# Kernel optimization log

Measured on AMD Instinct MI355X. Metric: run time of the kernel, lower is better.

## Reference

```python
import jax, jax.numpy as jnp
import numpy as np

DIM = 2048
DIM_HEAD = 64
NUM_HEADS = 32
FFN_INNER = 4 * DIM  # 8192
ATTN_INNER = NUM_HEADS * DIM_HEAD  # 2048
IN_WIDTH = FFN_INNER * 2 + 3 * ATTN_INNER  # 22528
OUT_IN = FFN_INNER + DIM  # 10240
B, S = 1, 2048


def setup_inputs() -> dict:
    key = jax.random.key(0)
    k0, k1, k2 = jax.random.split(key, 3)
    x = jax.random.normal(k0, (B, S, DIM), dtype=jnp.float32)
    W_in = jax.random.normal(k1, (DIM, IN_WIDTH), dtype=jnp.float32) * (DIM ** -0.5)
    W_out = jax.random.normal(k2, (OUT_IN, DIM), dtype=jnp.float32) * (OUT_IN ** -0.5)
    ln_w = jnp.ones((DIM,), dtype=jnp.float32)
    ln_b = jnp.zeros((DIM,), dtype=jnp.float32)
    return {"x": x, "ln_w": ln_w, "ln_b": ln_b, "W_in": W_in, "W_out": W_out}


def _layernorm(x, w, b, eps=1e-5):
    mu = jnp.mean(x, axis=-1, keepdims=True)
    var = jnp.mean(jnp.square(x - mu), axis=-1, keepdims=True)
    return (x - mu) * jax.lax.rsqrt(var + eps) * w + b


def reference(x, ln_w, ln_b, W_in, W_out):
    b, s, _ = x.shape
    h = _layernorm(x, ln_w, ln_b)
    res = h @ W_in  # [b, s, IN_WIDTH]
    q = res[..., :ATTN_INNER]
    k = res[..., ATTN_INNER:2 * ATTN_INNER]
    v = res[..., 2 * ATTN_INNER:3 * ATTN_INNER]
    ffn_input = res[..., 3 * ATTN_INNER:3 * ATTN_INNER + FFN_INNER]
    # b s (h d) -> b h s d
    q = q.reshape(b, s, NUM_HEADS, DIM_HEAD).transpose(0, 2, 1, 3)
    k = k.reshape(b, s, NUM_HEADS, DIM_HEAD).transpose(0, 2, 1, 3)
    v = v.reshape(b, s, NUM_HEADS, DIM_HEAD).transpose(0, 2, 1, 3)
    q = q * (DIM_HEAD ** -0.5)
    sim = jnp.einsum('bhsd,bhnd->bhsn', q, k)  # [b, h, s, s]
    causal = jnp.triu(jnp.ones((s, s), dtype=bool), k=1)
    sim = jnp.where(causal, -jnp.finfo(sim.dtype).max, sim)
    attn = jax.nn.softmax(sim, axis=-1)
    attn_out = jnp.einsum('bhsn,bhnd->bhsd', attn, v)
    attn_out = attn_out.transpose(0, 2, 1, 3).reshape(b, s, ATTN_INNER)
    concat_input = jnp.concatenate([attn_out, ffn_input], axis=-1)  # [b, s, OUT_IN]
    return concat_input @ W_out
```

## Files before the change

### kernel.cpp

```cpp
#include <hip/hip_runtime.h>
#include <stdint.h>

typedef __bf16 bf16x8 __attribute__((ext_vector_type(8)));
typedef float f32x4 __attribute__((ext_vector_type(4)));
typedef uint16_t u16x4 __attribute__((ext_vector_type(4)));
typedef uint16_t u16x8 __attribute__((ext_vector_type(8)));

#define LOG2E 1.4426950408889634f

__device__ __forceinline__ uint16_t f2bf(float f) {
  union { float f; uint32_t u; } v; v.f = f;
  return (uint16_t)((v.u + 0x7fffu + ((v.u >> 16) & 1u)) >> 16);
}

__device__ __forceinline__ void gload_lds16(const void* g, void* l) {
  __builtin_amdgcn_global_load_lds(
      (const __attribute__((address_space(1))) void*)g,
      (__attribute__((address_space(3))) void*)l, 16, 0, 0);
}

__device__ __forceinline__ f32x4 mfma16(bf16x8 a, bf16x8 b, f32x4 c) {
  return __builtin_amdgcn_mfma_f32_16x16x32_bf16(a, b, c, 0, 0, 0);
}

__global__ __launch_bounds__(256) void ln_kernel(const float* __restrict__ x,
                                                 const float* __restrict__ g,
                                                 const float* __restrict__ bta,
                                                 uint16_t* __restrict__ h) {
  const int row = blockIdx.x;
  const int t = threadIdx.x;
  const float* xr = x + (size_t)row * 2048 + t * 8;
  float4 v0 = *(const float4*)xr;
  float4 v1 = *(const float4*)(xr + 4);
  float s = v0.x + v0.y + v0.z + v0.w + v1.x + v1.y + v1.z + v1.w;
  float q = v0.x*v0.x + v0.y*v0.y + v0.z*v0.z + v0.w*v0.w
          + v1.x*v1.x + v1.y*v1.y + v1.z*v1.z + v1.w*v1.w;
  #pragma unroll
  for (int m = 1; m < 64; m <<= 1) {
    s += __shfl_xor(s, m);
    q += __shfl_xor(q, m);
  }
  __shared__ float ps[4], pq[4];
  const int wid = t >> 6, lane = t & 63;
  if (lane == 0) { ps[wid] = s; pq[wid] = q; }
  __syncthreads();
  s = ps[0] + ps[1] + ps[2] + ps[3];
  q = pq[0] + pq[1] + pq[2] + pq[3];
  const float mu = s * (1.0f / 2048.0f);
  const float var = q * (1.0f / 2048.0f) - mu * mu;
  const float rs = rsqrtf(var + 1e-5f);
  float4 w0 = *(const float4*)(g + t * 8);
  float4 w1 = *(const float4*)(g + t * 8 + 4);
  float4 b0 = *(const float4*)(bta + t * 8);
  float4 b1 = *(const float4*)(bta + t * 8 + 4);
  u16x8 o;
  o[0] = f2bf((v0.x - mu) * rs * w0.x + b0.x);
  o[1] = f2bf((v0.y - mu) * rs * w0.y + b0.y);
  o[2] = f2bf((v0.z - mu) * rs * w0.z + b0.z);
  o[3] = f2bf((v0.w - mu) * rs * w0.w + b0.w);
  o[4] = f2bf((v1.x - mu) * rs * w1.x + b1.x);
  o[5] = f2bf((v1.y - mu) * rs * w1.y + b1.y);
  o[6] = f2bf((v1.z - mu) * rs * w1.z + b1.z);
  o[7] = f2bf((v1.w - mu) * rs * w1.w + b1.w);
  *(u16x8*)(h + (size_t)row * 2048 + t * 8) = o;
}

__global__ __launch_bounds__(256) void transpose_w(const float* __restrict__ in,
                                                   uint16_t* __restrict__ out,
                                                   int R, int ldin,
                                                   int scale_cols, float scale) {
  __shared__ uint16_t tile[64][65];
  const int c0 = blockIdx.x * 64;
  const int r0 = blockIdx.y * 64;
  const int t = threadIdx.x;
  const int cc = (t & 15) * 4;
  const int rb = t >> 4;
  #pragma unroll
  for (int p = 0; p < 4; ++p) {
    const int r = rb + p * 16;
    const float4 v = *(const float4*)(in + (size_t)(r0 + r) * ldin + c0 + cc);
    const float m0 = (c0 + cc + 0) < scale_cols ? scale : 1.0f;
    const float m1 = (c0 + cc + 1) < scale_cols ? scale : 1.0f;
    const float m2 = (c0 + cc + 2) < scale_cols ? scale : 1.0f;
    const float m3 = (c0 + cc + 3) < scale_cols ? scale : 1.0f;
    tile[r][cc + 0] = f2bf(v.x * m0);
    tile[r][cc + 1] = f2bf(v.y * m1);
    tile[r][cc + 2] = f2bf(v.z * m2);
    tile[r][cc + 3] = f2bf(v.w * m3);
  }
  __syncthreads();
  #pragma unroll
  for (int p = 0; p < 4; ++p) {
    const int oc = rb + p * 16;
    u16x4 ov;
    ov.x = tile[cc + 0][oc];
    ov.y = tile[cc + 1][oc];
    ov.z = tile[cc + 2][oc];
    ov.w = tile[cc + 3][oc];
    *(u16x4*)(out + (size_t)(c0 + oc) * R + r0 + cc) = ov;
  }
}

__global__ __launch_bounds__(256) void transpose_v(const uint16_t* __restrict__ res,
                                                   uint16_t* __restrict__ vt) {
  __shared__ uint16_t tile[64][65];
  const int c0 = blockIdx.x * 64;
  const int r0 = blockIdx.y * 64;
  const int t = threadIdx.x;
  const int cc = (t & 15) * 4;
  const int rb = t >> 4;
  #pragma unroll
  for (int p = 0; p < 4; ++p) {
    const int r = rb + p * 16;
    const u16x4 v = *(const u16x4*)(res + (size_t)(r0 + r) * 14336 + 4096 + c0 + cc);
    tile[r][cc + 0] = v.x;
    tile[r][cc + 1] = v.y;
    tile[r][cc + 2] = v.z;
    tile[r][cc + 3] = v.w;
  }
  __syncthreads();
  #pragma unroll
  for (int p = 0; p < 4; ++p) {
    const int oc = rb + p * 16;
    u16x4 ov;
    ov.x = tile[cc + 0][oc];
    ov.y = tile[cc + 1][oc];
    ov.z = tile[cc + 2][oc];
    ov.w = tile[cc + 3][oc];
    *(u16x4*)(vt + (size_t)(c0 + oc) * 2048 + r0 + cc) = ov;
  }
}

template <int CONCAT, int CF32>
__global__ __launch_bounds__(512, 2) void gemm_pipe(
    const uint16_t* __restrict__ A0, const uint16_t* __restrict__ A1,
    const uint16_t* __restrict__ B, void* __restrict__ C0, void* __restrict__ C1,
    int ldbK, int ldc, int kchunk, int nt) {
  __shared__ __attribute__((aligned(16))) uint16_t Alds[4 * 256 * 32];
  __shared__ __attribute__((aligned(16))) uint16_t Blds[4 * 256 * 32];
  const int bid = blockIdx.x;
  const int q = gridDim.x >> 3;
  const int wg = (bid & 7) * q + (bid >> 3);
  const int m0 = (wg & 7) << 8;
  const int n0 = (wg >> 3) << 8;
  const int sk = blockIdx.y;
  const int k0 = sk * kchunk;
  const int t = threadIdx.x, wid = t >> 6, lane = t & 63;
  const int wr = wid >> 2, wc = wid & 3;

  f32x4 acc[8][4] = {};

  auto stage_tile = [&](int tt) {
    const int kg = k0 + tt * 32;
    const uint16_t* As; int lda, kc;
    if (CONCAT && kg >= 2048) { As = A1; lda = 14336; kc = kg + 4096; }
    else                      { As = A0; lda = 2048;  kc = kg; }
    const int slot = tt & 3;
    #pragma unroll
    for (int j = 0; j < 2; ++j) {
      const int chunk = (wid * 2 + j) * 64 + lane;
      const int r = chunk >> 2;
      const int s = (chunk & 3) ^ ((r >> 1) & 3);
      gload_lds16(As + (size_t)(m0 + r) * lda + kc + s * 8,
                  (char*)Alds + slot * 16384 + (wid * 2 + j) * 1024);
      gload_lds16(B + (size_t)(n0 + r) * ldbK + kg + s * 8,
                  (char*)Blds + slot * 16384 + (wid * 2 + j) * 1024);
    }
  };

  auto compute_tile = [&](int tt) {
    const int slot = tt & 3;
    const char* Ab = (const char*)Alds + slot * 16384;
    const char* Bb = (const char*)Blds + slot * 16384;
    bf16x8 af[8], bfv[4];
    #pragma unroll
    for (int m = 0; m < 8; ++m) {
      const int r = wr * 128 + m * 16 + (lane & 15);
      const int x = (lane >> 4) ^ ((r >> 1) & 3);
      af[m] = *(const bf16x8*)(Ab + r * 64 + x * 16);
    }
    #pragma unroll
    for (int n = 0; n < 4; ++n) {
      const int r = wc * 64 + n * 16 + (lane & 15);
      const int x = (lane >> 4) ^ ((r >> 1) & 3);
      bfv[n] = *(const bf16x8*)(Bb + r * 64 + x * 16);
    }
    #pragma unroll
    for (int m = 0; m < 8; ++m)
      #pragma unroll
      for (int n = 0; n < 4; ++n)
        acc[m][n] = mfma16(af[m], bfv[n], acc[m][n]);
  };

  stage_tile(0); stage_tile(1); stage_tile(2);
  for (int tt = 0; tt < nt; ++tt) {
    if (tt + 3 < nt) stage_tile(tt + 3);
    const int ahead = nt - 1 - tt;
    if (ahead >= 3)      asm volatile("s_waitcnt vmcnt(12)" ::: "memory");
    else if (ahead == 2) asm volatile("s_waitcnt vmcnt(8)" ::: "memory");
    else if (ahead == 1) asm volatile("s_waitcnt vmcnt(4)" ::: "memory");
    else                 asm volatile("s_waitcnt vmcnt(0)" ::: "memory");
    __builtin_amdgcn_s_barrier();
    __builtin_amdgcn_sched_barrier(0);
    compute_tile(tt);
    __builtin_amdgcn_s_barrier();
    __builtin_amdgcn_sched_barrier(0);
  }

  #pragma unroll
  for (int m = 0; m < 8; ++m)
    #pragma unroll
    for (int n = 0; n < 4; ++n)
      #pragma unroll
      for (int r = 0; r < 4; ++r) {
        const int row = m0 + wr * 128 + m * 16 + (lane >> 4) * 4 + r;
        const int col = n0 + wc * 64 + n * 16 + (lane & 15);
        if (CF32) {
          float* C = (sk == 0) ? (float*)C0
                               : ((float*)C1 + (size_t)(sk - 1) * 4194304ull);
          C[(size_t)row * ldc + col] = acc[m][n][r];
        } else {
          ((uint16_t*)C0)[(size_t)row * ldc + col] = f2bf(acc[m][n][r]);
        }
      }
}

__global__ __launch_bounds__(256) void reduce_add3(float* __restrict__ out,
                                                   const float* __restrict__ p) {
  const size_t i = ((size_t)blockIdx.x * 256 + threadIdx.x) * 4;
  float4 a = *(const float4*)(out + i);
  const float4 b = *(const float4*)(p + i);
  const float4 c = *(const float4*)(p + 4194304 + i);
  const float4 d = *(const float4*)(p + 8388608 + i);
  a.x += b.x + c.x + d.x;
  a.y += b.y + c.y + d.y;
  a.z += b.z + c.z + d.z;
  a.w += b.w + c.w + d.w;
  *(float4*)(out + i) = a;
}

__global__ __launch_bounds__(256) void attn_kernel(const uint16_t* __restrict__ res,
                                                   const uint16_t* __restrict__ vt,
                                                   uint16_t* __restrict__ aout) {
  const int qt = blockIdx.x;
  const int hh = blockIdx.y;
  const int q0 = qt * 128;
  const int t = threadIdx.x, wid = t >> 6, lane = t & 63;
  const int qw = q0 + wid * 32;
  __shared__ uint16_t Klds[64 * 64];
  __shared__ uint16_t Vlds[64 * 64];
  __shared__ uint16_t Plds[4 * 32 * 64];
  char* pbase = (char*)Plds + wid * 4096;

  bf16x8 qf[2][2];
  #pragma unroll
  for (int m = 0; m < 2; ++m)
    #pragma unroll
    for (int ks = 0; ks < 2; ++ks)
      qf[m][ks] = *(const bf16x8*)(res + (size_t)(qw + m * 16 + (lane & 15)) * 14336
                                   + hh * 64 + ks * 32 + (lane >> 4) * 8);
  f32x4 O[2][4] = {};
  f32x4 mrun[2], lrun[2];
  #pragma unroll
  for (int m = 0; m < 2; ++m)
    #pragma unroll
    for (int r = 0; r < 4; ++r) { mrun[m][r] = -1e30f; lrun[m][r] = 0.0f; }

  const int nkt = qt * 2 + 2;
  for (int kt = 0; kt < nkt; ++kt) {
    const int k0 = kt * 64;
    __syncthreads();
    #pragma unroll
    for (int i = 0; i < 2; ++i) {
      const int o = (wid * 2 + i) * 1024 + lane * 16;
      const int row = o >> 7;
      const int slot = (o >> 4) & 7;
      const int col = (slot ^ (row & 7)) << 3;
      gload_lds16(res + (size_t)(k0 + row) * 14336 + 2048 + hh * 64 + col,
                  (char*)Klds + (wid * 2 + i) * 1024);
      gload_lds16(vt + (size_t)(hh * 64 + row) * 2048 + k0 + col,
                  (char*)Vlds + (wid * 2 + i) * 1024);
    }
    __syncthreads();
    if (k0 <= qw + 31) {
      f32x4 s[2][4] = {};
      #pragma unroll
      for (int ks = 0; ks < 2; ++ks) {
        bf16x8 kf[4];
        #pragma unroll
        for (int n = 0; n < 4; ++n) {
          const int row = n * 16 + (lane & 15);
          const int slot = (ks * 4 + (lane >> 4)) ^ (row & 7);
          kf[n] = *(const bf16x8*)((const char*)Klds + row * 128 + slot * 16);
        }
        #pragma unroll
        for (int m = 0; m < 2; ++m)
          #pragma unroll
          for (int n = 0; n < 4; ++n)
            s[m][n] = mfma16(qf[m][ks], kf[n], s[m][n]);
      }
      if (k0 + 63 > qw) {
        #pragma unroll
        for (int m = 0; m < 2; ++m)
          #pragma unroll
          for (int n = 0; n < 4; ++n)
            #pragma unroll
            for (int r = 0; r < 4; ++r) {
              const int key = k0 + n * 16 + (lane & 15);
              const int qr = qw + m * 16 + (lane >> 4) * 4 + r;
              if (key > qr) s[m][n][r] = -1e30f;
            }
      }
      #pragma unroll
      for (int m = 0; m < 2; ++m) {
        f32x4 tmax = s[m][0];
        #pragma unroll
        for (int n = 1; n < 4; ++n)
          #pragma unroll
          for (int r = 0; r < 4; ++r) tmax[r] = fmaxf(tmax[r], s[m][n][r]);
        #pragma unroll
        for (int msk = 1; msk < 16; msk <<= 1)
          #pragma unroll
          for (int r = 0; r < 4; ++r) tmax[r] = fmaxf(tmax[r], __shfl_xor(tmax[r], msk));
        f32x4 newm, sc;
        #pragma unroll
        for (int r = 0; r < 4; ++r) {
          newm[r] = fmaxf(mrun[m][r], tmax[r]);
          sc[r] = exp2f((mrun[m][r] - newm[r]) * LOG2E);
          mrun[m][r] = newm[r];
        }
        f32x4 psum;
        #pragma unroll
        for (int r = 0; r < 4; ++r) psum[r] = 0.0f;
        #pragma unroll
        for (int n = 0; n < 4; ++n)
          #pragma unroll
          for (int r = 0; r < 4; ++r) {
            const float p = exp2f((s[m][n][r] - newm[r]) * LOG2E);
            s[m][n][r] = p;
            psum[r] += p;
          }
        #pragma unroll
        for (int msk = 1; msk < 16; msk <<= 1)
          #pragma unroll
          for (int r = 0; r < 4; ++r) psum[r] += __shfl_xor(psum[r], msk);
        #pragma unroll
        for (int r = 0; r < 4; ++r) lrun[m][r] = lrun[m][r] * sc[r] + psum[r];
        #pragma unroll
        for (int d = 0; d < 4; ++d)
          #pragma unroll
          for (int r = 0; r < 4; ++r) O[m][d][r] *= sc[r];
        #pragma unroll
        for (int n = 0; n < 4; ++n)
          #pragma unroll
          for (int r = 0; r < 4; ++r) {
            const int prow = m * 16 + (lane >> 4) * 4 + r;
            const int pcol = n * 16 + (lane & 15);
            *(uint16_t*)(pbase + prow * 128 + (((pcol >> 3) ^ (prow & 7)) << 4)
                         + (pcol & 7) * 2) = f2bf(s[m][n][r]);
          }
      }
      asm volatile("s_waitcnt lgkmcnt(0)" ::: "memory");
      #pragma unroll
      for (int ks = 0; ks < 2; ++ks) {
        bf16x8 pa[2], vf[4];
        #pragma unroll
        for (int m = 0; m < 2; ++m) {
          const int row = m * 16 + (lane & 15);
          const int slot = (ks * 4 + (lane >> 4)) ^ (row & 7);
          pa[m] = *(const bf16x8*)(pbase + row * 128 + slot * 16);
        }
        #pragma unroll
        for (int d = 0; d < 4; ++d) {
          const int row = d * 16 + (lane & 15);
          const int slot = (ks * 4 + (lane >> 4)) ^ (row & 7);
          vf[d] = *(const bf16x8*)((const char*)Vlds + row * 128 + slot * 16);
        }
        #pragma unroll
        for (int m = 0; m < 2; ++m)
          #pragma unroll
          for (int d = 0; d < 4; ++d)
            O[m][d] = mfma16(pa[m], vf[d], O[m][d]);
      }
    }
  }
  #pragma unroll
  for (int m = 0; m < 2; ++m) {
    f32x4 inv;
    #pragma unroll
    for (int r = 0; r < 4; ++r) inv[r] = 1.0f / lrun[m][r];
    #pragma unroll
    for (int d = 0; d < 4; ++d)
      #pragma unroll
      for (int r = 0; r < 4; ++r) {
        const int row = qw + m * 16 + (lane >> 4) * 4 + r;
        const int col = hh * 64 + d * 16 + (lane & 15);
        aout[(size_t)row * 2048 + col] = f2bf(O[m][d][r] * inv[r]);
      }
  }
}

extern "C" void kernel_launch(void* const* d_in, const int* in_sizes, int n_in,
                              void* d_out, int out_size, void* d_ws, size_t ws_size,
                              hipStream_t stream) {
  (void)in_sizes; (void)n_in; (void)out_size;
  const float* x     = (const float*)d_in[0];
  const float* ln_w  = (const float*)d_in[1];
  const float* ln_b  = (const float*)d_in[2];
  const float* W_in  = (const float*)d_in[3];
  const float* W_out = (const float*)d_in[4];

  const size_t need = 184549376ull;
  if (ws_size < need) return;
  char* ws = (char*)d_ws;
  size_t off = 0;
  uint16_t* h     = (uint16_t*)(ws + off); off += (size_t)2048 * 2048 * 2;
  uint16_t* WtIn  = (uint16_t*)(ws + off); off += (size_t)14336 * 2048 * 2;
  uint16_t* WtOut = (uint16_t*)(ws + off); off += (size_t)2048 * 10240 * 2;
  uint16_t* res   = (uint16_t*)(ws + off); off += (size_t)2048 * 14336 * 2;
  uint16_t* vt    = (uint16_t*)(ws + off); off += (size_t)2048 * 2048 * 2;
  uint16_t* aout  = (uint16_t*)(ws + off);
  float* partials = (float*)ws;

  ln_kernel<<<2048, 256, 0, stream>>>(x, ln_w, ln_b, h);
  transpose_w<<<dim3(224, 32), 256, 0, stream>>>(W_in, WtIn, 2048, 22528, 2048, 0.125f);
  transpose_w<<<dim3(32, 160), 256, 0, stream>>>(W_out, WtOut, 10240, 2048, 0, 1.0f);
  gemm_pipe<0, 0><<<dim3(448, 1), 512, 0, stream>>>(h, nullptr, WtIn, res, nullptr,
                                                    2048, 14336, 0, 64);
  transpose_v<<<dim3(32, 32), 256, 0, stream>>>(res, vt);
  attn_kernel<<<dim3(16, 32), 256, 0, stream>>>(res, vt, aout);
  gemm_pipe<1, 1><<<dim3(64, 4), 512, 0, stream>>>(aout, res, WtOut, d_out, partials,
                                                   10240, 2048, 2560, 80);
  reduce_add3<<<4096, 256, 0, stream>>>((float*)d_out, partials);
}
```

Before: 474.4 us.

## Restructure GEMM to 64-wide K tiles with double buffering and staggered loads

The bf16 GEMM kernel now loads 64-wide K tiles into two LDS buffers instead of 32-wide tiles into four. Each tile is split into four phases, and each phase interleaves one quarter of the next tiles' global-to-LDS loads with a slice of MFMA work under raised wave priority, with barriers between phases. The aim is to hide load latency behind compute while halving the number of loop iterations and reducing per-tile barrier overhead. In exchange it adds more barriers per tile and a shallower prefetch depth, and correctness depends on the vmcnt counting matching the new load issue order.

```diff
diff --git a/kernel.cpp b/kernel.cpp
--- a/kernel.cpp
+++ b/kernel.cpp
@@ -132,15 +132,15 @@
 }
 
 template <int CONCAT, int CF32>
-__global__ __launch_bounds__(512, 2) void gemm_pipe(
+__global__ __launch_bounds__(512, 2) void gemm_8p(
     const uint16_t* __restrict__ A0, const uint16_t* __restrict__ A1,
     const uint16_t* __restrict__ B, void* __restrict__ C0, void* __restrict__ C1,
     int ldbK, int ldc, int kchunk, int nt) {
-  __shared__ __attribute__((aligned(16))) uint16_t Alds[4 * 256 * 32];
-  __shared__ __attribute__((aligned(16))) uint16_t Blds[4 * 256 * 32];
+  __shared__ __attribute__((aligned(16))) uint16_t Alds[2 * 256 * 64];
+  __shared__ __attribute__((aligned(16))) uint16_t Blds[2 * 256 * 64];
   const int bid = blockIdx.x;
-  const int q = gridDim.x >> 3;
-  const int wg = (bid & 7) * q + (bid >> 3);
+  const int qx = gridDim.x >> 3;
+  const int wg = (bid & 7) * qx + (bid >> 3);
   const int m0 = (wg & 7) << 8;
   const int n0 = (wg >> 3) << 8;
   const int sk = blockIdx.y;
@@ -150,61 +150,84 @@
 
   f32x4 acc[8][4] = {};
 
-  auto stage_tile = [&](int tt) {
-    const int kg = k0 + tt * 32;
+  auto stageA = [&](int tt, int h) {
+    const int kg = k0 + tt * 64;
     const uint16_t* As; int lda, kc;
     if (CONCAT && kg >= 2048) { As = A1; lda = 14336; kc = kg + 4096; }
     else                      { As = A0; lda = 2048;  kc = kg; }
-    const int slot = tt & 3;
+    char* base = (char*)Alds + (tt & 1) * 32768 + h * 16384;
     #pragma unroll
     for (int j = 0; j < 2; ++j) {
-      const int chunk = (wid * 2 + j) * 64 + lane;
-      const int r = chunk >> 2;
-      const int s = (chunk & 3) ^ ((r >> 1) & 3);
-      gload_lds16(As + (size_t)(m0 + r) * lda + kc + s * 8,
-                  (char*)Alds + slot * 16384 + (wid * 2 + j) * 1024);
-      gload_lds16(B + (size_t)(n0 + r) * ldbK + kg + s * 8,
-                  (char*)Blds + slot * 16384 + (wid * 2 + j) * 1024);
+      const int chunk = j * 512 + t;
+      const int r = chunk >> 3, s = chunk & 7;
+      gload_lds16(As + (size_t)(m0 + h * 128 + r) * lda + kc + ((s ^ (r & 7)) << 3),
+                  base + chunk * 16);
     }
   };
-
-  auto compute_tile = [&](int tt) {
-    const int slot = tt & 3;
-    const char* Ab = (const char*)Alds + slot * 16384;
-    const char* Bb = (const char*)Blds + slot * 16384;
-    bf16x8 af[8], bfv[4];
-    #pragma unroll
-    for (int m = 0; m < 8; ++m) {
-      const int r = wr * 128 + m * 16 + (lane & 15);
-      const int x = (lane >> 4) ^ ((r >> 1) & 3);
-      af[m] = *(const bf16x8*)(Ab + r * 64 + x * 16);
+  auto stageB = [&](int tt, int h) {
+    const int kg = k0 + tt * 64;
+    char* base = (char*)Blds + (tt & 1) * 32768 + h * 16384;
+    #pragma unroll
+    for (int j = 0; j < 2; ++j) {
+      const int chunk = j * 512 + t;
+      const int r = chunk >> 3, s = chunk & 7;
+      gload_lds16(B + (size_t)(n0 + h * 128 + r) * ldbK + kg + ((s ^ (r & 7)) << 3),
+                  base + chunk * 16);
     }
-    #pragma unroll
-    for (int n = 0; n < 4; ++n) {
-      const int r = wc * 64 + n * 16 + (lane & 15);
-      const int x = (lane >> 4) ^ ((r >> 1) & 3);
-      bfv[n] = *(const bf16x8*)(Bb + r * 64 + x * 16);
+  };
+
+  stageB(0, 0); stageB(0, 1); stageA(0, 0); stageA(0, 1);
+  stageB(1, 0); stageB(1, 1);
+  asm volatile("s_waitcnt vmcnt(4)" ::: "memory");
+  __builtin_amdgcn_s_barrier();
+  __builtin_amdgcn_sched_barrier(0);
+
+  bf16x8 bf[4][2];
+  for (int tt = 0; tt < nt; ++tt) {
+    const char* Ab = (const char*)Alds + (tt & 1) * 32768;
+    const char* Bb = (const char*)Blds + (tt & 1) * 32768;
+    #pragma unroll
+    for (int q = 0; q < 4; ++q) {
+      if (q == 0) {
+        if (tt + 1 < nt) { asm volatile("s_waitcnt vmcnt(4)" ::: "memory"); }
+        else             { asm volatile("s_waitcnt vmcnt(0)" ::: "memory"); }
+        if (tt + 1 < nt) stageA(tt + 1, 0);
+        __builtin_amdgcn_s_barrier();
+        __builtin_amdgcn_sched_barrier(0);
+        #pragma unroll
+        for (int n = 0; n < 4; ++n)
+          #pragma unroll
+          for (int ks = 0; ks < 2; ++ks) {
+            const int r = wc * 64 + n * 16 + (lane & 15);
+            const int c = (ks * 4 + (lane >> 4)) ^ (r & 7);
+            bf[n][ks] = *(const bf16x8*)(Bb + r * 128 + c * 16);
+          }
+      } else {
+        if (q == 1)      { if (tt + 1 < nt) stageA(tt + 1, 1); }
+        else if (q == 2) { if (tt + 2 < nt) stageB(tt + 2, 0); }
+        else             { if (tt + 2 < nt) stageB(tt + 2, 1); }
+        __builtin_amdgcn_s_barrier();
+      }
+      bf16x8 af[2][2];
+      #pragma unroll
+      for (int i = 0; i < 2; ++i)
+        #pragma unroll
+        for (int ks = 0; ks < 2; ++ks) {
+          const int r = wr * 128 + (2 * q + i) * 16 + (lane & 15);
+          const int c = (ks * 4 + (lane >> 4)) ^ (r & 7);
+          af[i][ks] = *(const bf16x8*)(Ab + r * 128 + c * 16);
+        }
+      __builtin_amdgcn_s_setprio(1);
+      #pragma unroll
+      for (int i = 0; i < 2; ++i)
+        #pragma unroll
+        for (int n = 0; n < 4; ++n) {
+          acc[2 * q + i][n] = mfma16(af[i][0], bf[n][0], acc[2 * q + i][n]);
+          acc[2 * q + i][n] = mfma16(af[i][1], bf[n][1], acc[2 * q + i][n]);
+        }
+      __builtin_amdgcn_s_setprio(0);
+      __builtin_amdgcn_s_barrier();
     }
-    #pragma unroll
-    for (int m = 0; m < 8; ++m)
-      #pragma unroll
-      for (int n = 0; n < 4; ++n)
-        acc[m][n] = mfma16(af[m], bfv[n], acc[m][n]);
-  };
-
-  stage_tile(0); stage_tile(1); stage_tile(2);
-  for (int tt = 0; tt < nt; ++tt) {
-    if (tt + 3 < nt) stage_tile(tt + 3);
-    const int ahead = nt - 1 - tt;
-    if (ahead >= 3)      asm volatile("s_waitcnt vmcnt(12)" ::: "memory");
-    else if (ahead == 2) asm volatile("s_waitcnt vmcnt(8)" ::: "memory");
-    else if (ahead == 1) asm volatile("s_waitcnt vmcnt(4)" ::: "memory");
-    else                 asm volatile("s_waitcnt vmcnt(0)" ::: "memory");
-    __builtin_amdgcn_s_barrier();
-    __builtin_amdgcn_sched_barrier(0);
-    compute_tile(tt);
-    __builtin_amdgcn_s_barrier();
-    __builtin_amdgcn_sched_barrier(0);
   }
 
   #pragma unroll
@@ -425,11 +448,11 @@
   ln_kernel<<<2048, 256, 0, stream>>>(x, ln_w, ln_b, h);
   transpose_w<<<dim3(224, 32), 256, 0, stream>>>(W_in, WtIn, 2048, 22528, 2048, 0.125f);
   transpose_w<<<dim3(32, 160), 256, 0, stream>>>(W_out, WtOut, 10240, 2048, 0, 1.0f);
-  gemm_pipe<0, 0><<<dim3(448, 1), 512, 0, stream>>>(h, nullptr, WtIn, res, nullptr,
-                                                    2048, 14336, 0, 64);
+  gemm_8p<0, 0><<<dim3(448, 1), 512, 0, stream>>>(h, nullptr, WtIn, res, nullptr,
+                                                  2048, 14336, 0, 32);
   transpose_v<<<dim3(32, 32), 256, 0, stream>>>(res, vt);
   attn_kernel<<<dim3(16, 32), 256, 0, stream>>>(res, vt, aout);
-  gemm_pipe<1, 1><<<dim3(64, 4), 512, 0, stream>>>(aout, res, WtOut, d_out, partials,
-                                                   10240, 2048, 2560, 80);
+  gemm_8p<1, 1><<<dim3(64, 4), 512, 0, stream>>>(aout, res, WtOut, d_out, partials,
+                                                 10240, 2048, 2560, 40);
   reduce_add3<<<4096, 256, 0, stream>>>((float*)d_out, partials);
 }
```

Result: no change. 477.9 us (+0.7%).

## Split GEMM k-step into two half-phases interleaving LDS reads, staging and MFMA

Applied to the files above, without the earlier changes.

The GEMM main loop is restructured so each k-tile is processed in two halves of the M fragments. LDS fragment reads for one half and the staging of the next A or B tile are issued around MFMA bursts, and s_setprio raises wave priority during MFMA. The goal is to overlap global-to-LDS loads and LDS reads with matrix math instead of running them in serialized phases. The cost is extra barriers per iteration and more delicate vmcnt accounting.

```diff
diff --git a/kernel.cpp b/kernel.cpp
--- a/kernel.cpp
+++ b/kernel.cpp
@@ -132,15 +132,15 @@
 }
 
 template <int CONCAT, int CF32>
-__global__ __launch_bounds__(512, 2) void gemm_pipe(
+__global__ __launch_bounds__(512, 2) void gemm_fp(
     const uint16_t* __restrict__ A0, const uint16_t* __restrict__ A1,
     const uint16_t* __restrict__ B, void* __restrict__ C0, void* __restrict__ C1,
     int ldbK, int ldc, int kchunk, int nt) {
   __shared__ __attribute__((aligned(16))) uint16_t Alds[4 * 256 * 32];
   __shared__ __attribute__((aligned(16))) uint16_t Blds[4 * 256 * 32];
   const int bid = blockIdx.x;
-  const int q = gridDim.x >> 3;
-  const int wg = (bid & 7) * q + (bid >> 3);
+  const int qx = gridDim.x >> 3;
+  const int wg = (bid & 7) * qx + (bid >> 3);
   const int m0 = (wg & 7) << 8;
   const int n0 = (wg >> 3) << 8;
   const int sk = blockIdx.y;
@@ -149,60 +149,88 @@
   const int wr = wid >> 2, wc = wid & 3;
 
   f32x4 acc[8][4] = {};
-
-  auto stage_tile = [&](int tt) {
+  bf16x8 bfr[4];
+
+  auto stageA = [&](int tt) {
     const int kg = k0 + tt * 32;
     const uint16_t* As; int lda, kc;
     if (CONCAT && kg >= 2048) { As = A1; lda = 14336; kc = kg + 4096; }
     else                      { As = A0; lda = 2048;  kc = kg; }
-    const int slot = tt & 3;
+    char* abase = (char*)Alds + (tt & 3) * 16384;
     #pragma unroll
     for (int j = 0; j < 2; ++j) {
-      const int chunk = (wid * 2 + j) * 64 + lane;
-      const int r = chunk >> 2;
-      const int s = (chunk & 3) ^ ((r >> 1) & 3);
-      gload_lds16(As + (size_t)(m0 + r) * lda + kc + s * 8,
-                  (char*)Alds + slot * 16384 + (wid * 2 + j) * 1024);
-      gload_lds16(B + (size_t)(n0 + r) * ldbK + kg + s * 8,
-                  (char*)Blds + slot * 16384 + (wid * 2 + j) * 1024);
+      const int ch = j * 512 + t;
+      const int r = ch >> 2, s = ch & 3;
+      gload_lds16(As + (size_t)(m0 + r) * lda + kc + ((s ^ ((r >> 1) & 3)) << 3),
+                  abase + ch * 16);
     }
   };
-
-  auto compute_tile = [&](int tt) {
-    const int slot = tt & 3;
-    const char* Ab = (const char*)Alds + slot * 16384;
-    const char* Bb = (const char*)Blds + slot * 16384;
-    bf16x8 af[8], bfv[4];
-    #pragma unroll
-    for (int m = 0; m < 8; ++m) {
-      const int r = wr * 128 + m * 16 + (lane & 15);
-      const int x = (lane >> 4) ^ ((r >> 1) & 3);
-      af[m] = *(const bf16x8*)(Ab + r * 64 + x * 16);
-    }
+  auto stageB = [&](int tt) {
+    const int kg = k0 + tt * 32;
+    char* bbase = (char*)Blds + (tt & 3) * 16384;
+    #pragma unroll
+    for (int j = 0; j < 2; ++j) {
+      const int ch = j * 512 + t;
+      const int r = ch >> 2, s = ch & 3;
+      gload_lds16(B + (size_t)(n0 + r) * ldbK + kg + ((s ^ ((r >> 1) & 3)) << 3),
+                  bbase + ch * 16);
+    }
+  };
+
+  auto ldA = [&](int buf, int half, bf16x8 af[4]) {
+    const char* Ab = (const char*)Alds + buf * 16384;
+    #pragma unroll
+    for (int i = 0; i < 4; ++i) {
+      const int r = wr * 128 + (half * 4 + i) * 16 + (lane & 15);
+      const int c = (lane >> 4) ^ ((r >> 1) & 3);
+      af[i] = *(const bf16x8*)(Ab + r * 64 + c * 16);
+    }
+  };
+  auto ldB = [&](int buf) {
+    const char* Bb = (const char*)Blds + buf * 16384;
     #pragma unroll
     for (int n = 0; n < 4; ++n) {
       const int r = wc * 64 + n * 16 + (lane & 15);
-      const int x = (lane >> 4) ^ ((r >> 1) & 3);
-      bfv[n] = *(const bf16x8*)(Bb + r * 64 + x * 16);
-    }
-    #pragma unroll
-    for (int m = 0; m < 8; ++m)
+      const int c = (lane >> 4) ^ ((r >> 1) & 3);
+      bfr[n] = *(const bf16x8*)(Bb + r * 64 + c * 16);
+    }
+  };
+  auto MF = [&](int half, bf16x8 af[4]) {
+    __builtin_amdgcn_s_setprio(1);
+    #pragma unroll
+    for (int i = 0; i < 4; ++i)
       #pragma unroll
       for (int n = 0; n < 4; ++n)
-        acc[m][n] = mfma16(af[m], bfv[n], acc[m][n]);
+        acc[half * 4 + i][n] = mfma16(af[i], bfr[n], acc[half * 4 + i][n]);
+    __builtin_amdgcn_s_setprio(0);
   };
 
-  stage_tile(0); stage_tile(1); stage_tile(2);
+  stageA(0); stageB(0); stageA(1); stageB(1); stageA(2); stageB(2);
+  asm volatile("s_waitcnt vmcnt(8)" ::: "memory");
+  __builtin_amdgcn_s_barrier();
+  __builtin_amdgcn_sched_barrier(0);
+
   for (int tt = 0; tt < nt; ++tt) {
-    if (tt + 3 < nt) stage_tile(tt + 3);
-    const int ahead = nt - 1 - tt;
-    if (ahead >= 3)      asm volatile("s_waitcnt vmcnt(12)" ::: "memory");
-    else if (ahead == 2) asm volatile("s_waitcnt vmcnt(8)" ::: "memory");
-    else if (ahead == 1) asm volatile("s_waitcnt vmcnt(4)" ::: "memory");
-    else                 asm volatile("s_waitcnt vmcnt(0)" ::: "memory");
+    const int buf = tt & 3;
+    bf16x8 afA[4], afB[4];
+    ldB(buf);
+    ldA(buf, 0, afA);
+    if (tt + 3 < nt) stageA(tt + 3);
+    __builtin_amdgcn_s_barrier();
+    asm volatile("s_waitcnt lgkmcnt(0)" ::: "memory");
+    __builtin_amdgcn_sched_barrier(0);
+    MF(0, afA);
     __builtin_amdgcn_s_barrier();
     __builtin_amdgcn_sched_barrier(0);
-    compute_tile(tt);
+    ldA(buf, 1, afB);
+    if (tt + 3 < nt) stageB(tt + 3);
+    if (tt + 3 < nt)      { asm volatile("s_waitcnt vmcnt(8)" ::: "memory"); }
+    else if (tt + 2 < nt) { asm volatile("s_waitcnt vmcnt(4)" ::: "memory"); }
+    else if (tt + 1 < nt) { asm volatile("s_waitcnt vmcnt(0)" ::: "memory"); }
+    __builtin_amdgcn_s_barrier();
+    asm volatile("s_waitcnt lgkmcnt(0)" ::: "memory");
+    __builtin_amdgcn_sched_barrier(0);
+    MF(1, afB);
     __builtin_amdgcn_s_barrier();
     __builtin_amdgcn_sched_barrier(0);
   }
@@ -425,11 +453,11 @@
   ln_kernel<<<2048, 256, 0, stream>>>(x, ln_w, ln_b, h);
   transpose_w<<<dim3(224, 32), 256, 0, stream>>>(W_in, WtIn, 2048, 22528, 2048, 0.125f);
   transpose_w<<<dim3(32, 160), 256, 0, stream>>>(W_out, WtOut, 10240, 2048, 0, 1.0f);
-  gemm_pipe<0, 0><<<dim3(448, 1), 512, 0, stream>>>(h, nullptr, WtIn, res, nullptr,
-                                                    2048, 14336, 0, 64);
+  gemm_fp<0, 0><<<dim3(448, 1), 512, 0, stream>>>(h, nullptr, WtIn, res, nullptr,
+                                                  2048, 14336, 0, 64);
   transpose_v<<<dim3(32, 32), 256, 0, stream>>>(res, vt);
   attn_kernel<<<dim3(16, 32), 256, 0, stream>>>(res, vt, aout);
-  gemm_pipe<1, 1><<<dim3(64, 4), 512, 0, stream>>>(aout, res, WtOut, d_out, partials,
-                                                   10240, 2048, 2560, 80);
+  gemm_fp<1, 1><<<dim3(64, 4), 512, 0, stream>>>(aout, res, WtOut, d_out, partials,
+                                                 10240, 2048, 2560, 80);
   reduce_add3<<<4096, 256, 0, stream>>>((float*)d_out, partials);
 }
```

Result: faster. 443.9 us (-6.4%).

## Shrink GEMM tiles to 256x128 with 4 waves and double-buffered LDS

Applied to the files above, without the earlier changes.

Replaces the 512-thread 256x256 GEMM block, which used a 4-stage LDS pipeline, with a 256-thread 256x128 block using two LDS buffers and a single barrier per k-step. Each wave keeps the same 128x64 accumulator footprint, and the grids double to cover the output. The smaller LDS footprint and block size are meant to allow more blocks per CU and cut barrier overhead. In exchange, prefetch depth drops from 3 tiles to 1, so memory latency may be exposed, and B-operand reuse per block is halved.

```diff
diff --git a/kernel.cpp b/kernel.cpp
--- a/kernel.cpp
+++ b/kernel.cpp
@@ -132,78 +132,74 @@
 }
 
 template <int CONCAT, int CF32>
-__global__ __launch_bounds__(512, 2) void gemm_pipe(
+__global__ __launch_bounds__(256, 2) void gemm_tb(
     const uint16_t* __restrict__ A0, const uint16_t* __restrict__ A1,
     const uint16_t* __restrict__ B, void* __restrict__ C0, void* __restrict__ C1,
     int ldbK, int ldc, int kchunk, int nt) {
-  __shared__ __attribute__((aligned(16))) uint16_t Alds[4 * 256 * 32];
-  __shared__ __attribute__((aligned(16))) uint16_t Blds[4 * 256 * 32];
+  __shared__ __attribute__((aligned(16))) uint16_t Alds[2][256 * 32];
+  __shared__ __attribute__((aligned(16))) uint16_t Blds[2][128 * 32];
   const int bid = blockIdx.x;
-  const int q = gridDim.x >> 3;
-  const int wg = (bid & 7) * q + (bid >> 3);
+  const int qx = gridDim.x >> 3;
+  const int wg = (bid & 7) * qx + (bid >> 3);
   const int m0 = (wg & 7) << 8;
-  const int n0 = (wg >> 3) << 8;
+  const int n0 = (wg >> 3) << 7;
   const int sk = blockIdx.y;
   const int k0 = sk * kchunk;
   const int t = threadIdx.x, wid = t >> 6, lane = t & 63;
-  const int wr = wid >> 2, wc = wid & 3;
+  const int wr = wid >> 1, wc = wid & 1;
 
   f32x4 acc[8][4] = {};
 
-  auto stage_tile = [&](int tt) {
+  auto stage = [&](int tt) {
     const int kg = k0 + tt * 32;
     const uint16_t* As; int lda, kc;
     if (CONCAT && kg >= 2048) { As = A1; lda = 14336; kc = kg + 4096; }
     else                      { As = A0; lda = 2048;  kc = kg; }
-    const int slot = tt & 3;
+    char* ab = (char*)Alds[tt & 1];
+    char* bb = (char*)Blds[tt & 1];
+    #pragma unroll
+    for (int j = 0; j < 4; ++j) {
+      const int ch = j * 256 + t;
+      const int r = ch >> 2, s = ch & 3;
+      gload_lds16(As + (size_t)(m0 + r) * lda + kc + ((s ^ ((r >> 1) & 3)) << 3),
+                  ab + ch * 16);
+    }
     #pragma unroll
     for (int j = 0; j < 2; ++j) {
-      const int chunk = (wid * 2 + j) * 64 + lane;
-      const int r = chunk >> 2;
-      const int s = (chunk & 3) ^ ((r >> 1) & 3);
-      gload_lds16(As + (size_t)(m0 + r) * lda + kc + s * 8,
-                  (char*)Alds + slot * 16384 + (wid * 2 + j) * 1024);
-      gload_lds16(B + (size_t)(n0 + r) * ldbK + kg + s * 8,
-                  (char*)Blds + slot * 16384 + (wid * 2 + j) * 1024);
+      const int ch = j * 256 + t;
+      const int r = ch >> 2, s = ch & 3;
+      gload_lds16(B + (size_t)(n0 + r) * ldbK + kg + ((s ^ ((r >> 1) & 3)) << 3),
+                  bb + ch * 16);
     }
   };
 
-  auto compute_tile = [&](int tt) {
-    const int slot = tt & 3;
-    const char* Ab = (const char*)Alds + slot * 16384;
-    const char* Bb = (const char*)Blds + slot * 16384;
-    bf16x8 af[8], bfv[4];
+  stage(0);
+  for (int tt = 0; tt < nt; ++tt) {
+    const int buf = tt & 1;
+    asm volatile("s_waitcnt vmcnt(0)" ::: "memory");
+    __builtin_amdgcn_s_barrier();
+    __builtin_amdgcn_sched_barrier(0);
+    if (tt + 1 < nt) stage(tt + 1);
+    const char* Ab = (const char*)Alds[buf];
+    const char* Bb = (const char*)Blds[buf];
+    bf16x8 bfr[4], af[8];
+    #pragma unroll
+    for (int n = 0; n < 4; ++n) {
+      const int r = wc * 64 + n * 16 + (lane & 15);
+      const int c = (lane >> 4) ^ ((r >> 1) & 3);
+      bfr[n] = *(const bf16x8*)(Bb + r * 64 + c * 16);
+    }
     #pragma unroll
     for (int m = 0; m < 8; ++m) {
       const int r = wr * 128 + m * 16 + (lane & 15);
-      const int x = (lane >> 4) ^ ((r >> 1) & 3);
-      af[m] = *(const bf16x8*)(Ab + r * 64 + x * 16);
-    }
-    #pragma unroll
-    for (int n = 0; n < 4; ++n) {
-      const int r = wc * 64 + n * 16 + (lane & 15);
-      const int x = (lane >> 4) ^ ((r >> 1) & 3);
-      bfv[n] = *(const bf16x8*)(Bb + r * 64 + x * 16);
+      const int c = (lane >> 4) ^ ((r >> 1) & 3);
+      af[m] = *(const bf16x8*)(Ab + r * 64 + c * 16);
     }
     #pragma unroll
     for (int m = 0; m < 8; ++m)
       #pragma unroll
       for (int n = 0; n < 4; ++n)
-        acc[m][n] = mfma16(af[m], bfv[n], acc[m][n]);
-  };
-
-  stage_tile(0); stage_tile(1); stage_tile(2);
-  for (int tt = 0; tt < nt; ++tt) {
-    if (tt + 3 < nt) stage_tile(tt + 3);
-    const int ahead = nt - 1 - tt;
-    if (ahead >= 3)      asm volatile("s_waitcnt vmcnt(12)" ::: "memory");
-    else if (ahead == 2) asm volatile("s_waitcnt vmcnt(8)" ::: "memory");
-    else if (ahead == 1) asm volatile("s_waitcnt vmcnt(4)" ::: "memory");
-    else                 asm volatile("s_waitcnt vmcnt(0)" ::: "memory");
-    __builtin_amdgcn_s_barrier();
-    __builtin_amdgcn_sched_barrier(0);
-    compute_tile(tt);
-    __builtin_amdgcn_s_barrier();
+        acc[m][n] = mfma16(af[m], bfr[n], acc[m][n]);
     __builtin_amdgcn_sched_barrier(0);
   }
 
@@ -425,11 +421,11 @@
   ln_kernel<<<2048, 256, 0, stream>>>(x, ln_w, ln_b, h);
   transpose_w<<<dim3(224, 32), 256, 0, stream>>>(W_in, WtIn, 2048, 22528, 2048, 0.125f);
   transpose_w<<<dim3(32, 160), 256, 0, stream>>>(W_out, WtOut, 10240, 2048, 0, 1.0f);
-  gemm_pipe<0, 0><<<dim3(448, 1), 512, 0, stream>>>(h, nullptr, WtIn, res, nullptr,
-                                                    2048, 14336, 0, 64);
+  gemm_tb<0, 0><<<dim3(896, 1), 256, 0, stream>>>(h, nullptr, WtIn, res, nullptr,
+                                                  2048, 14336, 0, 64);
   transpose_v<<<dim3(32, 32), 256, 0, stream>>>(res, vt);
   attn_kernel<<<dim3(16, 32), 256, 0, stream>>>(res, vt, aout);
-  gemm_pipe<1, 1><<<dim3(64, 4), 512, 0, stream>>>(aout, res, WtOut, d_out, partials,
-                                                   10240, 2048, 2560, 80);
+  gemm_tb<1, 1><<<dim3(128, 4), 256, 0, stream>>>(aout, res, WtOut, d_out, partials,
+                                                  10240, 2048, 2560, 80);
   reduce_add3<<<4096, 256, 0, stream>>>((float*)d_out, partials);
 }
```

After: 454.1 us. 1.04x faster.
